# Kernel optimization log

Measured on AMD Instinct MI355X. Metric: run time of the kernel, lower is better.

Reference implementation:

```python
import jax, jax.numpy as jnp
import numpy as np

LOC = 200 * 200 + 1   # location vocab
E = 100               # loc_emb_size
H = 100               # hidden_neurons (== input size of STLSTM)
D = 12                # temporal/spatial slot embedding dim
NSLOT = 92


def setup_inputs() -> dict:
    key = jax.random.key(0)
    ks = jax.random.split(key, 24)
    B, T = 1024, 256
    inp = {}
    inp["traj"] = jax.random.randint(ks[0], (B, T), 0, LOC)
    inp["lennew"] = jax.random.randint(ks[1], (B, T), 0, T)
    inp["traj_len"] = 255  # static scalar (loop runs traj_len+1 steps)
    inp["tu"] = jax.random.randint(ks[2], (B, T), 0, NSLOT)
    inp["tl"] = jax.random.randint(ks[3], (B, T), 0, NSLOT)
    inp["tu_slot"] = jax.random.randint(ks[4], (B, T), 0, NSLOT)
    inp["tl_slot"] = jax.random.randint(ks[5], (B, T), 0, NSLOT)
    inp["su"] = jax.random.randint(ks[6], (B, T), 0, NSLOT)
    inp["sl"] = jax.random.randint(ks[7], (B, T), 0, NSLOT)
    inp["su_slot"] = jax.random.randint(ks[8], (B, T), 0, NSLOT)
    inp["sl_slot"] = jax.random.randint(ks[9], (B, T), 0, NSLOT)
    # learned parameters
    inp["emb_loc"] = jax.random.normal(ks[10], (LOC, E), jnp.float32) * 0.02
    inp["emb_t"] = jax.random.normal(ks[11], (NSLOT, D), jnp.float32) * 0.02
    inp["emb_s"] = jax.random.normal(ks[12], (NSLOT, D), jnp.float32) * 0.02
    inp["W_ih"] = jax.random.normal(ks[13], (E, 4 * H), jnp.float32) * 0.05
    inp["W_hh"] = jax.random.normal(ks[14], (H, 4 * H), jnp.float32) * 0.05
    inp["b"] = jnp.zeros((4 * H,), jnp.float32)
    inp["W_xt"] = jax.random.normal(ks[15], (E, H), jnp.float32) * 0.05
    inp["W_tt"] = jax.random.normal(ks[16], (D, H), jnp.float32) * 0.05
    inp["b_t"] = jnp.zeros((H,), jnp.float32)
    inp["W_xs"] = jax.random.normal(ks[17], (E, H), jnp.float32) * 0.05
    inp["W_ss"] = jax.random.normal(ks[18], (D, H), jnp.float32) * 0.05
    inp["b_s"] = jnp.zeros((H,), jnp.float32)
    return inp


def reference(traj, lennew, traj_len, tu, tl, tu_slot, tl_slot, su, sl,
              su_slot, sl_slot, emb_loc, emb_t, emb_s, W_ih, W_hh, b,
              W_xt, W_tt, b_t, W_xs, W_ss, b_s):
    steps = int(traj_len) + 1  # static python int -> static slice
    x = emb_loc[traj[:, :steps]]            # [B, S, E] (dropout is identity in eval)
    dtype = x.dtype

    def interp(up_e, low_e, up_d, low_d):
        # linear interpolation between upper/lower slot embeddings
        up = up_d[:, :steps].astype(dtype)[..., None]
        low = low_d[:, :steps].astype(dtype)[..., None]
        return (up * low_e + low * up_e) / jnp.maximum(up + low, 1.0)

    Tq = interp(emb_t[tu[:, :steps]], emb_t[tl[:, :steps]], tu_slot, tl_slot)  # [B,S,D]
    Sq = interp(emb_s[su[:, :steps]], emb_s[sl[:, :steps]], su_slot, sl_slot)  # [B,S,D]

    B = traj.shape[0]
    h0 = jnp.zeros((B, H), dtype)
    c0 = jnp.zeros((B, H), dtype)
    xs = (x.swapaxes(0, 1), Tq.swapaxes(0, 1), Sq.swapaxes(0, 1))  # time-major

    def step(carry, inp):
        h, c = carry
        xt, tg, sg = inp
        gates = xt @ W_ih + h @ W_hh + b           # [B, 4H]
        i, f, g, o = jnp.split(gates, 4, axis=-1)
        i = jax.nn.sigmoid(i)
        f = jax.nn.sigmoid(f)
        g = jnp.tanh(g)
        o = jax.nn.sigmoid(o)
        tgate = jax.nn.sigmoid(xt @ W_xt + tg @ W_tt + b_t)  # temporal gate
        sgate = jax.nn.sigmoid(xt @ W_xs + sg @ W_ss + b_s)  # spatial gate
        c = f * c + i * tgate * sgate * g
        h = o * jnp.tanh(c)
        return (h, c), None

    (h, c), _ = jax.lax.scan(step, (h0, c0), xs)
    # model returns h at index traj_len, which is the final hidden state
    return h
```

## Files before the change

### kernel.cpp

```cpp
#include <hip/hip_runtime.h>

#define B_    1024
#define T_    256
#define LOCN  40001
#define E_    100
#define H_    100
#define NC    600

__device__ __forceinline__ float fsig(float x) {
    const float e = __builtin_amdgcn_exp2f(x * -1.442695040888963f);
    return __builtin_amdgcn_rcpf(1.f + e);
}

constexpr int PROWS = 16;
constexpr int PPAD  = 20;

__global__ __launch_bounds__(320) void proj_loc_kernel(
    const float* __restrict__ emb_loc,
    const float* __restrict__ W_ih,
    const float* __restrict__ W_xt,
    const float* __restrict__ W_xs,
    const float* __restrict__ b,
    const float* __restrict__ b_t,
    const float* __restrict__ b_s,
    float* __restrict__ P)
{
    __shared__ __attribute__((aligned(16))) float aT[E_][PPAD];
    const int tid  = threadIdx.x;
    const int row0 = blockIdx.x * PROWS;

    for (int i = tid; i < PROWS * E_; i += 320) {
        int r = i / E_, k = i - r * E_;
        int rr = row0 + r;
        float v = 0.f;
        if (rr < LOCN) v = emb_loc[rr * E_ + k];
        aT[k][r] = v;
    }
    __syncthreads();
    if (tid >= 300) return;

    for (int cc = 0; cc < 2; ++cc) {
        const int c = tid + cc * 300;
        const float* wp; int stride; float bias;
        if (c < 400)      { wp = W_ih + c;         stride = 400; bias = b[c]; }
        else if (c < 500) { wp = W_xt + (c - 400); stride = 100; bias = b_t[c - 400]; }
        else              { wp = W_xs + (c - 500); stride = 100; bias = b_s[c - 500]; }

        float acc[PROWS];
        #pragma unroll
        for (int r = 0; r < PROWS; ++r) acc[r] = bias;

        for (int k = 0; k < E_; ++k) {
            float w = wp[(size_t)k * stride];
            #pragma unroll
            for (int r = 0; r < PROWS; ++r) acc[r] += aT[k][r] * w;
        }
        #pragma unroll
        for (int r = 0; r < PROWS; ++r) {
            int rr = row0 + r;
            if (rr < LOCN) P[(size_t)rr * NC + c] = acc[r];
        }
    }
}

__global__ void proj_ts_kernel(
    const float* __restrict__ emb_t, const float* __restrict__ emb_s,
    const float* __restrict__ W_tt,  const float* __restrict__ W_ss,
    float* __restrict__ P_t, float* __restrict__ P_s)
{
    int idx = blockIdx.x * 256 + threadIdx.x;
    if (idx >= 2 * 92 * H_) return;
    int which = idx / (92 * H_);
    int rem   = idx - which * (92 * H_);
    int r = rem / H_, c = rem - r * H_;
    const float* e = which ? emb_s : emb_t;
    const float* W = which ? W_ss : W_tt;
    float acc = 0.f;
    #pragma unroll
    for (int k = 0; k < 12; ++k) acc += e[r * 12 + k] * W[k * H_ + c];
    (which ? P_s : P_t)[rem] = acc;
}

constexpr int RB = 4;
constexpr int NT = 704;

__global__ __launch_bounds__(NT, 3) void lstm_rec_kernel(
    const int* __restrict__ traj,
    const int* __restrict__ traj_len_p,
    const int* __restrict__ tu,      const int* __restrict__ tl,
    const int* __restrict__ tu_slot, const int* __restrict__ tl_slot,
    const int* __restrict__ su,      const int* __restrict__ sl,
    const int* __restrict__ su_slot, const int* __restrict__ sl_slot,
    const float* __restrict__ P,
    const float* __restrict__ P_t,
    const float* __restrict__ P_s,
    const float* __restrict__ W_hh,
    float* __restrict__ out)
{
    __shared__ __attribute__((aligned(16))) float h_lds[RB][H_];
    __shared__ float gates_lds[RB][400];
    __shared__ float tg_lds[RB][H_];
    __shared__ float sg_lds[RB][H_];
    __shared__ int   loc_lds[2][RB];

    const int tid = threadIdx.x;
    const int b0  = blockIdx.x * RB;
    int steps = traj_len_p[0] + 1;
    if (steps > T_) steps = T_;

    float w[H_];
    if (tid < 400) {
        #pragma unroll
        for (int k = 0; k < H_; ++k) w[k] = W_hh[k * 400 + tid];
        ((float*)h_lds)[tid] = 0.f;
    }
    if (tid < RB) loc_lds[0][tid] = traj[(b0 + tid) * T_];

    const int er = tid / 100;
    const int eh = tid - er * 100;
    float c_reg = 0.f, hval = 0.f;
    __syncthreads();

    for (int t = 0; t < steps; ++t) {
        const int buf = t & 1;

        if (tid >= 700) {
            int r = tid - 700;
            if (t + 1 < steps) loc_lds[buf ^ 1][r] = traj[(b0 + r) * T_ + t + 1];
        }

        if (tid < 400) {
            const int n = tid;
            float gacc[RB];
            #pragma unroll
            for (int r = 0; r < RB; ++r) {
                const int loc = __builtin_amdgcn_readfirstlane(loc_lds[buf][r]);
                const float* __restrict__ Prow = P + (size_t)loc * NC;
                gacc[r] = Prow[n];
            }

            float acc[RB] = {0.f, 0.f, 0.f, 0.f};
            #pragma unroll
            for (int k4 = 0; k4 < H_ / 4; ++k4) {
                #pragma unroll
                for (int r = 0; r < RB; ++r) {
                    float4 hv = *(const float4*)(&h_lds[r][k4 * 4]);
                    acc[r] += hv.x * w[k4 * 4 + 0];
                    acc[r] += hv.y * w[k4 * 4 + 1];
                    acc[r] += hv.z * w[k4 * 4 + 2];
                    acc[r] += hv.w * w[k4 * 4 + 3];
                }
            }
            const bool isg = (n >= 200 && n < 300);
            #pragma unroll
            for (int r = 0; r < RB; ++r) {
                float v  = acc[r] + gacc[r];
                float xx = isg ? 2.f * v : v;
                float s  = fsig(xx);
                gates_lds[r][n] = isg ? (2.f * s - 1.f) : s;
            }
        }

        if (tid >= 448 && tid < 648) {
            const int  ch   = tid - 448;
            const bool is_t = ch < 100;
            const int  hx   = is_t ? ch : ch - 100;
            const int* up_a = is_t ? tu_slot : su_slot;
            const int* lo_a = is_t ? tl_slot : sl_slot;
            const int* ui_a = is_t ? tu : su;
            const int* li_a = is_t ? tl : sl;
            const float* Pq = is_t ? P_t : P_s;
            float* dst      = is_t ? &tg_lds[0][0] : &sg_lds[0][0];
            #pragma unroll
            for (int r = 0; r < RB; ++r) {
                const int off = __builtin_amdgcn_readfirstlane((b0 + r) * T_ + t);
                const int loc = __builtin_amdgcn_readfirstlane(loc_lds[buf][r]);
                const float* __restrict__ Prow = P + (size_t)loc * NC;
                float gp  = Prow[400 + ch];
                float up  = (float)up_a[off];
                float low = (float)lo_a[off];
                int   ui  = ui_a[off], li = li_a[off];
                const float inv = __builtin_amdgcn_rcpf(fmaxf(up + low, 1.f));
                float iv  = (up * Pq[li * H_ + hx] + low * Pq[ui * H_ + hx]) * inv;
                float pre = gp + iv;
                dst[r * H_ + hx] = fsig(pre);
            }
        }
        __syncthreads();

        if (tid < 400) {
            float i_g = gates_lds[er][eh];
            float f_g = gates_lds[er][100 + eh];
            float g_g = gates_lds[er][200 + eh];
            float o_g = gates_lds[er][300 + eh];
            float tsg = tg_lds[er][eh] * sg_lds[er][eh];
            c_reg = f_g * c_reg + i_g * tsg * g_g;
            hval  = o_g * (2.f * fsig(2.f * c_reg) - 1.f);
            h_lds[er][eh] = hval;
        }
        __syncthreads();
    }

    if (tid < 400) out[b0 * H_ + tid] = hval;
}

extern "C" void kernel_launch(void* const* d_in, const int* in_sizes, int n_in,
                              void* d_out, int out_size, void* d_ws, size_t ws_size,
                              hipStream_t stream) {
    const int*   traj     = (const int*)  d_in[0];
    const int*   traj_len = (const int*)  d_in[2];
    const int*   tu       = (const int*)  d_in[3];
    const int*   tl       = (const int*)  d_in[4];
    const int*   tu_slot  = (const int*)  d_in[5];
    const int*   tl_slot  = (const int*)  d_in[6];
    const int*   su       = (const int*)  d_in[7];
    const int*   sl       = (const int*)  d_in[8];
    const int*   su_slot  = (const int*)  d_in[9];
    const int*   sl_slot  = (const int*)  d_in[10];
    const float* emb_loc  = (const float*)d_in[11];
    const float* emb_t    = (const float*)d_in[12];
    const float* emb_s    = (const float*)d_in[13];
    const float* W_ih     = (const float*)d_in[14];
    const float* W_hh     = (const float*)d_in[15];
    const float* b        = (const float*)d_in[16];
    const float* W_xt     = (const float*)d_in[17];
    const float* W_tt     = (const float*)d_in[18];
    const float* b_t      = (const float*)d_in[19];
    const float* W_xs     = (const float*)d_in[20];
    const float* W_ss     = (const float*)d_in[21];
    const float* b_s      = (const float*)d_in[22];

    float* P   = (float*)d_ws;
    float* P_t = P + (size_t)LOCN * NC;
    float* P_s = P_t + 92 * H_;

    proj_loc_kernel<<<(LOCN + PROWS - 1) / PROWS, 320, 0, stream>>>(
        emb_loc, W_ih, W_xt, W_xs, b, b_t, b_s, P);
    proj_ts_kernel<<<(2 * 92 * H_ + 255) / 256, 256, 0, stream>>>(
        emb_t, emb_s, W_tt, W_ss, P_t, P_s);
    lstm_rec_kernel<<<B_ / RB, NT, 0, stream>>>(
        traj, traj_len, tu, tl, tu_slot, tl_slot, su, sl, su_slot, sl_slot,
        P, P_t, P_s, W_hh, (float*)d_out);
}
```

Measured before the change: 774.0 us.

## Prefetch next-step gate inputs into registers and relax per-step barriers

The recurrent loop now issues the global loads for step t+1 (the projected-gate rows and the temporal/spatial interpolation operands) during step t and holds them in registers. Location indices are staged two steps ahead in the double-buffered LDS array. Each `__syncthreads` is replaced by an inline barrier that waits only on LDS counters, so outstanding global loads can stay in flight across the barrier. The aim is to take global-memory latency off the serial per-step critical path, at the cost of more registers and reliance on hand-written barrier semantics.

```diff
diff --git a/kernel.cpp b/kernel.cpp
--- a/kernel.cpp
+++ b/kernel.cpp
@@ -114,10 +114,49 @@
         for (int k = 0; k < H_; ++k) w[k] = W_hh[k * 400 + tid];
         ((float*)h_lds)[tid] = 0.f;
     }
-    if (tid < RB) loc_lds[0][tid] = traj[(b0 + tid) * T_];
+
+    const bool isTS = (tid >= 448 && tid < 648);
+    const int  ch   = tid - 448;
+    const bool is_t = ch < 100;
+    const int  hx   = is_t ? ch : ch - 100;
+    const int* up_a = is_t ? tu_slot : su_slot;
+    const int* lo_a = is_t ? tl_slot : sl_slot;
+    const int* ui_a = is_t ? tu : su;
+    const int* li_a = is_t ? tl : sl;
+    const float* Pq = is_t ? P_t : P_s;
+    const int  gcol = (is_t ? 400 : 500) + hx;
+    float* dst      = is_t ? &tg_lds[0][0] : &sg_lds[0][0];
 
     const int er = tid / 100;
     const int eh = tid - er * 100;
+
+    float gacc_cur[RB];
+    float ts_up[RB], ts_lo[RB], ts_gp[RB], ts_pql[RB], ts_pqu[RB];
+
+    if (tid < 400) {
+        #pragma unroll
+        for (int r = 0; r < RB; ++r) {
+            const int loc0 = __builtin_amdgcn_readfirstlane(traj[(b0 + r) * T_]);
+            gacc_cur[r] = P[(size_t)loc0 * NC + tid];
+        }
+    }
+    if (isTS) {
+        #pragma unroll
+        for (int r = 0; r < RB; ++r) {
+            const int off0 = __builtin_amdgcn_readfirstlane((b0 + r) * T_);
+            const int loc0 = __builtin_amdgcn_readfirstlane(traj[off0]);
+            ts_up[r] = (float)up_a[off0];
+            ts_lo[r] = (float)lo_a[off0];
+            const int ui = ui_a[off0], li = li_a[off0];
+            ts_gp[r]  = P[(size_t)loc0 * NC + gcol];
+            ts_pql[r] = Pq[li * H_ + hx];
+            ts_pqu[r] = Pq[ui * H_ + hx];
+        }
+    }
+    if (tid < RB) {
+        const int t1 = (steps > 1) ? 1 : 0;
+        loc_lds[1][tid] = traj[(b0 + tid) * T_ + t1];
+    }
     float c_reg = 0.f, hval = 0.f;
     __syncthreads();
 
@@ -125,20 +164,19 @@
         const int buf = t & 1;
 
         if (tid >= 700) {
-            int r = tid - 700;
-            if (t + 1 < steps) loc_lds[buf ^ 1][r] = traj[(b0 + r) * T_ + t + 1];
+            const int r  = tid - 700;
+            const int t2 = (t + 2 < steps) ? t + 2 : steps - 1;
+            loc_lds[buf][r] = traj[(b0 + r) * T_ + t2];
         }
 
         if (tid < 400) {
             const int n = tid;
-            float gacc[RB];
-            #pragma unroll
-            for (int r = 0; r < RB; ++r) {
-                const int loc = __builtin_amdgcn_readfirstlane(loc_lds[buf][r]);
-                const float* __restrict__ Prow = P + (size_t)loc * NC;
-                gacc[r] = Prow[n];
-            }
-
+            float gacc_nxt[RB];
+            #pragma unroll
+            for (int r = 0; r < RB; ++r) {
+                const int locN = __builtin_amdgcn_readfirstlane(loc_lds[buf ^ 1][r]);
+                gacc_nxt[r] = P[(size_t)locN * NC + n];
+            }
             float acc[RB] = {0.f, 0.f, 0.f, 0.f};
             #pragma unroll
             for (int k4 = 0; k4 < H_ / 4; ++k4) {
@@ -154,39 +192,36 @@
             const bool isg = (n >= 200 && n < 300);
             #pragma unroll
             for (int r = 0; r < RB; ++r) {
-                float v  = acc[r] + gacc[r];
+                float v  = acc[r] + gacc_cur[r];
                 float xx = isg ? 2.f * v : v;
                 float s  = fsig(xx);
                 gates_lds[r][n] = isg ? (2.f * s - 1.f) : s;
             }
-        }
-
-        if (tid >= 448 && tid < 648) {
-            const int  ch   = tid - 448;
-            const bool is_t = ch < 100;
-            const int  hx   = is_t ? ch : ch - 100;
-            const int* up_a = is_t ? tu_slot : su_slot;
-            const int* lo_a = is_t ? tl_slot : sl_slot;
-            const int* ui_a = is_t ? tu : su;
-            const int* li_a = is_t ? tl : sl;
-            const float* Pq = is_t ? P_t : P_s;
-            float* dst      = is_t ? &tg_lds[0][0] : &sg_lds[0][0];
-            #pragma unroll
-            for (int r = 0; r < RB; ++r) {
-                const int off = __builtin_amdgcn_readfirstlane((b0 + r) * T_ + t);
-                const int loc = __builtin_amdgcn_readfirstlane(loc_lds[buf][r]);
-                const float* __restrict__ Prow = P + (size_t)loc * NC;
-                float gp  = Prow[400 + ch];
-                float up  = (float)up_a[off];
-                float low = (float)lo_a[off];
-                int   ui  = ui_a[off], li = li_a[off];
-                const float inv = __builtin_amdgcn_rcpf(fmaxf(up + low, 1.f));
-                float iv  = (up * Pq[li * H_ + hx] + low * Pq[ui * H_ + hx]) * inv;
-                float pre = gp + iv;
-                dst[r * H_ + hx] = fsig(pre);
-            }
-        }
-        __syncthreads();
+            #pragma unroll
+            for (int r = 0; r < RB; ++r) gacc_cur[r] = gacc_nxt[r];
+        }
+
+        if (isTS) {
+            #pragma unroll
+            for (int r = 0; r < RB; ++r) {
+                const float inv = __builtin_amdgcn_rcpf(fmaxf(ts_up[r] + ts_lo[r], 1.f));
+                const float iv  = (ts_up[r] * ts_pql[r] + ts_lo[r] * ts_pqu[r]) * inv;
+                dst[r * H_ + hx] = fsig(ts_gp[r] + iv);
+            }
+            const int tn = (t + 1 < steps) ? t + 1 : steps - 1;
+            #pragma unroll
+            for (int r = 0; r < RB; ++r) {
+                const int offN = __builtin_amdgcn_readfirstlane((b0 + r) * T_ + tn);
+                const int locN = __builtin_amdgcn_readfirstlane(loc_lds[buf ^ 1][r]);
+                ts_up[r] = (float)up_a[offN];
+                ts_lo[r] = (float)lo_a[offN];
+                const int ui = ui_a[offN], li = li_a[offN];
+                ts_gp[r]  = P[(size_t)locN * NC + gcol];
+                ts_pql[r] = Pq[li * H_ + hx];
+                ts_pqu[r] = Pq[ui * H_ + hx];
+            }
+        }
+        asm volatile("s_waitcnt lgkmcnt(0)\n\ts_barrier" ::: "memory");
 
         if (tid < 400) {
             float i_g = gates_lds[er][eh];
@@ -198,7 +233,7 @@
             hval  = o_g * (2.f * fsig(2.f * c_reg) - 1.f);
             h_lds[er][eh] = hval;
         }
-        __syncthreads();
+        asm volatile("s_waitcnt lgkmcnt(0)\n\ts_barrier" ::: "memory");
     }
 
     if (tid < 400) out[b0 * H_ + tid] = hval;
```

Result: slower. 1.251 ms (+61.6%).
